# Performance work log

Hardware: AMD Instinct MI355X
Metric: run time of the kernel (lower is better)

Reference implementation:

```python
import jax, jax.numpy as jnp
import numpy as np

B, N, M = 8, 8192, 1024
C1, C2 = 256, 512
C_IN, C_MID, C_OUT = 768, 256, 256  # mlp = [768, 256, 256]
EPS_BN = 1e-5
EPS_W = 1e-8


def setup_inputs() -> dict:
    key = jax.random.key(0)
    ks = jax.random.split(key, 10)
    inp = {
        "unknown": jax.random.uniform(ks[0], (B, N, 3), dtype=jnp.float32),
        "known": jax.random.uniform(ks[1], (B, M, 3), dtype=jnp.float32),
        "unknow_feats": jax.random.normal(ks[2], (B, C1, N), dtype=jnp.float32),
        "known_feats": jax.random.normal(ks[3], (B, C2, M), dtype=jnp.float32),
        # conv1d (kernel=1) weights, bias-free (followed by BN), per create_convblock1d
        "W1": jax.random.normal(ks[4], (C_MID, C_IN), dtype=jnp.float32) * (1.0 / np.sqrt(C_IN)),
        "g1": jnp.ones((C_MID,), jnp.float32),
        "b1": jnp.zeros((C_MID,), jnp.float32),
        "W2": jax.random.normal(ks[5], (C_OUT, C_MID), dtype=jnp.float32) * (1.0 / np.sqrt(C_MID)),
        "g2": jnp.ones((C_OUT,), jnp.float32),
        "b2": jnp.zeros((C_OUT,), jnp.float32),
    }
    return inp


def _three_interpolation(unknown, known, known_feats):
    # squared pairwise distances (B, N, M), as in pointnet2 three_nn CUDA kernel
    d2 = jnp.sum((unknown[:, :, None, :] - known[:, None, :, :]) ** 2, axis=-1)
    neg_d, idx = jax.lax.top_k(-d2, 3)            # (B, N, 3)
    dist = -neg_d
    w = 1.0 / (dist + EPS_W)
    w = w / jnp.sum(w, axis=-1, keepdims=True)    # (B, N, 3)
    gathered = jax.vmap(lambda f, i: f[:, i])(known_feats, idx)  # (B, C2, N, 3)
    return jnp.einsum("bcnk,bnk->bcn", gathered, w)              # (B, C2, N)


def _conv_bn_relu(x, W, g, b):
    # 1x1 conv1d (no bias) + BatchNorm1d (training-mode stats) + ReLU
    y = jnp.einsum("oc,bcn->bon", W, x)
    mean = jnp.mean(y, axis=(0, 2), keepdims=True)
    var = jnp.var(y, axis=(0, 2), keepdims=True)
    y = (y - mean) * jax.lax.rsqrt(var + EPS_BN)
    y = y * g[None, :, None] + b[None, :, None]
    return jax.nn.relu(y)


def reference(unknown, known, unknow_feats, known_feats, W1, g1, b1, W2, g2, b2):
    interp = _three_interpolation(unknown, known, known_feats)   # (B, C2, N)
    new_features = jnp.concatenate([unknow_feats, interp], axis=1)  # (B, C1+C2, N)
    h = _conv_bn_relu(new_features, W1, g1, b1)
    out = _conv_bn_relu(h, W2, g2, b2)
    return out  # (B, C_OUT, N)
```

## Files before the change

kernel.cpp:

```cpp
#include <hip/hip_runtime.h>

#define B_    8
#define N_    8192
#define M_    1024
#define C1_   256
#define C2_   512
#define CIN_  768
#define CMID_ 256
#define COUT_ 256

typedef __attribute__((ext_vector_type(8))) __bf16 bf16x8;
typedef __attribute__((ext_vector_type(4))) float f32x4;
typedef __attribute__((ext_vector_type(4))) unsigned short u16x4;
typedef __attribute__((ext_vector_type(8))) unsigned short u16x8;

__device__ __forceinline__ unsigned short f2bf(float f) {
  union { float f; unsigned u; } v; v.f = f;
  unsigned r = v.u + 0x7FFFu + ((v.u >> 16) & 1u);
  return (unsigned short)(r >> 16);
}
__device__ __forceinline__ float bf2f(unsigned short h) {
  union { unsigned u; float f; } v; v.u = ((unsigned)h) << 16; return v.f;
}

__device__ __forceinline__ void gload16(const void* g, void* l) {
  __builtin_amdgcn_global_load_lds((const __attribute__((address_space(1))) unsigned int*)g,
                                   (__attribute__((address_space(3))) unsigned int*)l, 16, 0, 0);
}


__global__ void k_cast(const float* __restrict__ in, unsigned short* __restrict__ out, int n) {
  int i = blockIdx.x * 256 + threadIdx.x;
  if (i < n) out[i] = f2bf(in[i]);
}

__global__ void k_tr_kf(const float* __restrict__ in, float* __restrict__ out) {
  __shared__ float t[32][33];
  int b = blockIdx.z;
  int c0 = blockIdx.x * 32, m0 = blockIdx.y * 32;
  int tx = threadIdx.x, ty = threadIdx.y;
  const float* ip = in + ((size_t)b * C2_ + c0) * M_ + m0;
#pragma unroll
  for (int i = 0; i < 32; i += 8) t[ty + i][tx] = ip[(size_t)(ty + i) * M_ + tx];
  __syncthreads();
  float* op = out + ((size_t)b * M_ + m0) * C2_ + c0;
#pragma unroll
  for (int i = 0; i < 32; i += 8) op[(size_t)(ty + i) * C2_ + tx] = t[tx][ty + i];
}

__global__ void k_tr_uf(const float* __restrict__ in, unsigned short* __restrict__ out) {
  __shared__ float t[32][33];
  int b = blockIdx.z;
  int c0 = blockIdx.x * 32, n0 = blockIdx.y * 32;
  int tx = threadIdx.x, ty = threadIdx.y;
  const float* ip = in + ((size_t)b * C1_ + c0) * N_ + n0;
#pragma unroll
  for (int i = 0; i < 32; i += 8) t[ty + i][tx] = ip[(size_t)(ty + i) * N_ + tx];
  __syncthreads();
  unsigned short* op = out + ((size_t)b * N_ + n0) * CIN_ + c0;
#pragma unroll
  for (int i = 0; i < 32; i += 8) op[(size_t)(ty + i) * CIN_ + tx] = f2bf(t[tx][ty + i]);
}


__device__ __forceinline__ void ins3(float db, int ib, float& d0, int& i0,
                                     float& d1, int& i1, float& d2, int& i2) {
  if (db < d2 || (db == d2 && ib < i2)) {
    if (db < d1 || (db == d1 && ib < i1)) {
      d2 = d1; i2 = i1;
      if (db < d0 || (db == d0 && ib < i0)) { d1 = d0; i1 = i0; d0 = db; i0 = ib; }
      else                                  { d1 = db; i1 = ib; }
    } else { d2 = db; i2 = ib; }
  }
}

__global__ __launch_bounds__(256) void k_three_nn(const float* __restrict__ unknown,
                                                  const float* __restrict__ known,
                                                  int* __restrict__ idx, float* __restrict__ wgt) {
  __shared__ __align__(16) float kpts[M_][4];
  int b = blockIdx.x >> 8;
  int n0 = (blockIdx.x & 255) << 5;
  for (int i = threadIdx.x; i < M_; i += 256) {
    const float* kp = known + ((size_t)b * M_ + i) * 3;
    kpts[i][0] = kp[0]; kpts[i][1] = kp[1]; kpts[i][2] = kp[2];
  }
  __syncthreads();
  const int l = threadIdx.x & 63;
  const int j = l & 7;
  const int q = ((threadIdx.x >> 6) << 3) + (l >> 3);
  const int n = n0 + q;
  const float* up = unknown + ((size_t)b * N_ + n) * 3;
  float ux = up[0], uy = up[1], uz = up[2];
  float d0 = 1e30f, d1 = 1e30f, d2v = 1e30f;
  int i0 = 0, i1 = 0, i2 = 0;
  for (int t = 0; t < 128; ++t) {
    int i = t * 8 + j;
    f32x4 p = *(const f32x4*)kpts[i];
    float dx = __fsub_rn(ux, p[0]);
    float dy = __fsub_rn(uy, p[1]);
    float dz = __fsub_rn(uz, p[2]);
    float d = __fadd_rn(__fadd_rn(__fmul_rn(dx, dx), __fmul_rn(dy, dy)), __fmul_rn(dz, dz));
    if (d < d2v) {
      if (d < d1) {
        if (d < d0) { d2v = d1; i2 = i1; d1 = d0; i1 = i0; d0 = d; i0 = i; }
        else        { d2v = d1; i2 = i1; d1 = d;  i1 = i; }
      } else        { d2v = d;  i2 = i; }
    }
  }
#pragma unroll
  for (int m = 1; m <= 4; m <<= 1) {
    float e0 = __shfl_xor(d0, m), e1 = __shfl_xor(d1, m), e2 = __shfl_xor(d2v, m);
    int   f0 = __shfl_xor(i0, m), f1 = __shfl_xor(i1, m), f2 = __shfl_xor(i2, m);
    ins3(e0, f0, d0, i0, d1, i1, d2v, i2);
    ins3(e1, f1, d0, i0, d1, i1, d2v, i2);
    ins3(e2, f2, d0, i0, d1, i1, d2v, i2);
  }
  if (j == 0) {
    float w0 = 1.f / (d0 + 1e-8f), w1 = 1.f / (d1 + 1e-8f), w2 = 1.f / (d2v + 1e-8f);
    float s = w0 + w1 + w2;
    size_t base = ((size_t)b * N_ + n) * 3;
    idx[base] = i0; idx[base + 1] = i1; idx[base + 2] = i2;
    wgt[base] = w0 / s; wgt[base + 1] = w1 / s; wgt[base + 2] = w2 / s;
  }
}

__global__ __launch_bounds__(256) void k_interp(const float* __restrict__ kft, const int* __restrict__ idx,
                                                const float* __restrict__ wgt, unsigned short* __restrict__ xt) {
  int pb = blockIdx.x * 8 + (threadIdx.x >> 5);
  int lane = threadIdx.x & 31;
  int b = pb >> 13;
  size_t t3 = (size_t)pb * 3;
  int i0 = idx[t3], i1 = idx[t3 + 1], i2 = idx[t3 + 2];
  float w0 = wgt[t3], w1 = wgt[t3 + 1], w2 = wgt[t3 + 2];
  const f32x4* f0 = (const f32x4*)(kft + ((size_t)b * M_ + i0) * C2_);
  const f32x4* f1 = (const f32x4*)(kft + ((size_t)b * M_ + i1) * C2_);
  const f32x4* f2 = (const f32x4*)(kft + ((size_t)b * M_ + i2) * C2_);
  unsigned short* o = xt + (size_t)pb * CIN_ + C1_;
#pragma unroll
  for (int k = 0; k < 4; ++k) {
    int c4 = lane + 32 * k;
    f32x4 a = f0[c4], bb = f1[c4], cc = f2[c4];
    u16x4 r;
#pragma unroll
    for (int e = 0; e < 4; ++e) r[e] = f2bf(w0 * a[e] + w1 * bb[e] + w2 * cc[e]);
    *(u16x4*)(o + 4 * c4) = r;
  }
}


template <int K, int EPI, bool BN>
__global__ __launch_bounds__(256) void gemm_bt(const unsigned short* __restrict__ A,
                                               const unsigned short* __restrict__ Bm,
                                               unsigned short* __restrict__ C,
                                               float* __restrict__ psum, float* __restrict__ psq,
                                               const float* __restrict__ scale,
                                               const float* __restrict__ shift) {
  __shared__ __align__(16) char lds[32768];
  __shared__ float lsc[256], lsh[256];
  const int tid = threadIdx.x;
  const int l = tid & 63;
  const int wv = tid >> 6;
  const int wr = wv >> 1, wc = wv & 1;
  const int b = blockIdx.z;
  const int o0 = blockIdx.y * 128;
  const int n0 = blockIdx.x * 128;
  const char* Ab = (const char*)A + (size_t)o0 * (K * 2);
  const char* Bb = (const char*)Bm + ((size_t)b * N_ + n0) * (K * 2);

  if (BN) { lsc[tid] = scale[tid]; lsh[tid] = shift[tid]; }

  f32x4 zero = {0.f, 0.f, 0.f, 0.f};
  f32x4 acc[4][4];
#pragma unroll
  for (int i = 0; i < 4; ++i)
#pragma unroll
    for (int j = 0; j < 4; ++j) acc[i][j] = zero;

  const int grow = wv * 32 + (l >> 3);
  const int gcol = (((l & 7) ^ (l >> 3)) * 16);
  int srow[4], scol[4];
#pragma unroll
  for (int i = 0; i < 4; ++i) { int q = tid + i * 256; srow[i] = q >> 3; scol[i] = (q & 7) * 16; }

  bf16x8 rb[4];
  if (BN) {
#pragma unroll
    for (int i = 0; i < 4; ++i)
      rb[i] = *(const bf16x8*)(Bb + (size_t)srow[i] * (K * 2) + scol[i]);
  }

  const int NK = K / 64;
  for (int kt = 0; kt < NK; ++kt) {
    __syncthreads();
#pragma unroll
    for (int i = 0; i < 4; ++i) {
      int r = grow + i * 8;
      gload16(Ab + (size_t)r * (K * 2) + kt * 128 + gcol, lds + wv * 4096 + i * 1024);
      if (!BN)
        gload16(Bb + (size_t)r * (K * 2) + kt * 128 + gcol, lds + 16384 + wv * 4096 + i * 1024);
    }
    if (BN) {
#pragma unroll
      for (int i = 0; i < 4; ++i) {
        u16x8 v = *(u16x8*)&rb[i];
        u16x8 r;
        int c0 = kt * 64 + (scol[i] >> 1);
#pragma unroll
        for (int e = 0; e < 8; ++e) {
          float f = bf2f(v[e]) * lsc[c0 + e] + lsh[c0 + e];
          r[e] = f2bf(fmaxf(f, 0.f));
        }
        *(u16x8*)(lds + 16384 + srow[i] * 128 + (scol[i] ^ ((srow[i] & 7) << 4))) = r;
      }
    }
    __syncthreads();
    if (BN && kt + 1 < NK) {
      const char* Bk = Bb + (size_t)(kt + 1) * 128;
#pragma unroll
      for (int i = 0; i < 4; ++i)
        rb[i] = *(const bf16x8*)(Bk + (size_t)srow[i] * (K * 2) + scol[i]);
    }
#pragma unroll
    for (int kk = 0; kk < 2; ++kk) {
      bf16x8 af[4], bfr[4];
#pragma unroll
      for (int mi = 0; mi < 4; ++mi) {
        int row = wr * 64 + mi * 16 + (l & 15);
        int cb = (kk * 64 + ((l >> 4) * 16)) ^ ((row & 7) << 4);
        af[mi] = *(const bf16x8*)(lds + row * 128 + cb);
      }
#pragma unroll
      for (int ni = 0; ni < 4; ++ni) {
        int row = wc * 64 + ni * 16 + (l & 15);
        int cb = (kk * 64 + ((l >> 4) * 16)) ^ ((row & 7) << 4);
        bfr[ni] = *(const bf16x8*)(lds + 16384 + row * 128 + cb);
      }
#pragma unroll
      for (int mi = 0; mi < 4; ++mi)
#pragma unroll
        for (int ni = 0; ni < 4; ++ni)
          acc[mi][ni] = __builtin_amdgcn_mfma_f32_16x16x32_bf16(af[mi], bfr[ni], acc[mi][ni], 0, 0, 0);
    }
  }

#pragma unroll
  for (int mi = 0; mi < 4; ++mi) {
    int o = o0 + wr * 64 + mi * 16 + ((l >> 4) << 2);
#pragma unroll
    for (int ni = 0; ni < 4; ++ni) {
      int n = n0 + wc * 64 + ni * 16 + (l & 15);
      if (EPI == 0) {
        u16x4 pk;
#pragma unroll
        for (int r = 0; r < 4; ++r) pk[r] = f2bf(acc[mi][ni][r]);
        *(u16x4*)(C + ((size_t)b * N_ + n) * 256 + o) = pk;
      } else {
#pragma unroll
        for (int r = 0; r < 4; ++r)
          C[((size_t)b * 256 + (o + r)) * N_ + n] = f2bf(acc[mi][ni][r]);
      }
    }
  }

  const int slot = (blockIdx.z * 64 + blockIdx.x) * 2 + wc;
#pragma unroll
  for (int mi = 0; mi < 4; ++mi) {
    float s[4] = {0.f, 0.f, 0.f, 0.f}, q[4] = {0.f, 0.f, 0.f, 0.f};
#pragma unroll
    for (int ni = 0; ni < 4; ++ni)
#pragma unroll
      for (int r = 0; r < 4; ++r) { float v = acc[mi][ni][r]; s[r] += v; q[r] = fmaf(v, v, q[r]); }
#pragma unroll
    for (int m = 1; m <= 8; m <<= 1)
#pragma unroll
      for (int r = 0; r < 4; ++r) { s[r] += __shfl_xor(s[r], m); q[r] += __shfl_xor(q[r], m); }
    if ((l & 15) == 0) {
      int o = o0 + wr * 64 + mi * 16 + ((l >> 4) << 2);
#pragma unroll
      for (int r = 0; r < 4; ++r) {
        psum[(size_t)(o + r) * 1024 + slot] = s[r];
        psq [(size_t)(o + r) * 1024 + slot] = q[r];
      }
    }
  }
}


__global__ __launch_bounds__(256) void k_finalize(const float* __restrict__ psum,
                                                  const float* __restrict__ psq,
                                                  const float* __restrict__ g,
                                                  const float* __restrict__ bb,
                                                  float* __restrict__ scale,
                                                  float* __restrict__ shift) {
  int c = blockIdx.x;
  const float* ps = psum + (size_t)c * 1024;
  const float* pq = psq + (size_t)c * 1024;
  float s = 0.f, q = 0.f;
#pragma unroll
  for (int k = 0; k < 4; ++k) { s += ps[threadIdx.x + 256 * k]; q += pq[threadIdx.x + 256 * k]; }
#pragma unroll
  for (int off = 32; off; off >>= 1) { s += __shfl_down(s, off); q += __shfl_down(q, off); }
  __shared__ float rs[4], rq[4];
  if ((threadIdx.x & 63) == 0) { rs[threadIdx.x >> 6] = s; rq[threadIdx.x >> 6] = q; }
  __syncthreads();
  if (threadIdx.x == 0) {
    float S = rs[0] + rs[1] + rs[2] + rs[3];
    float Q = rq[0] + rq[1] + rq[2] + rq[3];
    const float inv_n = 1.f / 65536.f;
    float mean = S * inv_n;
    float var = Q * inv_n - mean * mean;
    float rstd = rsqrtf(var + 1e-5f);
    float sc = g[c] * rstd;
    scale[c] = sc;
    shift[c] = bb[c] - mean * sc;
  }
}

__global__ void k_bnrelu_out(const unsigned short* __restrict__ y, const float* __restrict__ scale,
                             const float* __restrict__ shift, float* __restrict__ out) {
  size_t i = ((size_t)blockIdx.x * 256 + threadIdx.x) * 4;
  int c = (int)((i >> 13) & 255);
  float sc = scale[c], sh = shift[c];
  u16x4 v = *(const u16x4*)(y + i);
  f32x4 o;
#pragma unroll
  for (int k = 0; k < 4; ++k) o[k] = fmaxf(bf2f(v[k]) * sc + sh, 0.f);
  *(f32x4*)(out + i) = o;
}


extern "C" void kernel_launch(void* const* d_in, const int* in_sizes, int n_in,
                              void* d_out, int out_size, void* d_ws, size_t ws_size,
                              hipStream_t stream) {
  const float* unknown = (const float*)d_in[0];
  const float* known   = (const float*)d_in[1];
  const float* uf      = (const float*)d_in[2];
  const float* kf      = (const float*)d_in[3];
  const float* W1      = (const float*)d_in[4];
  const float* g1      = (const float*)d_in[5];
  const float* b1      = (const float*)d_in[6];
  const float* W2      = (const float*)d_in[7];
  const float* g2      = (const float*)d_in[8];
  const float* b2      = (const float*)d_in[9];
  float* out = (float*)d_out;

  char* ws = (char*)d_ws;
  unsigned short* xt  = (unsigned short*)(ws);
  unsigned short* y1  = (unsigned short*)(ws + 100663296);
  unsigned short* y2  = (unsigned short*)(ws + 134217728);
  float*          kft = (float*)(ws + 167772160);
  float*          psum = (float*)(ws + 167772160);
  float*          psq  = (float*)(ws + 168820736);
  unsigned short* w1b = (unsigned short*)(ws + 184549376);
  unsigned short* w2b = (unsigned short*)(ws + 184942592);
  int*            idx = (int*)(ws + 185073664);
  float*          wgt = (float*)(ws + 185860096);
  float*          st  = (float*)(ws + 186646528);
  float *sc1 = st, *sh1 = st + 256, *sc2 = st + 512, *sh2 = st + 768;

  k_cast<<<768, 256, 0, stream>>>(W1, w1b, CMID_ * CIN_);
  k_cast<<<256, 256, 0, stream>>>(W2, w2b, COUT_ * CMID_);
  k_tr_kf<<<dim3(16, 32, B_), dim3(32, 8), 0, stream>>>(kf, kft);
  k_tr_uf<<<dim3(8, 256, B_), dim3(32, 8), 0, stream>>>(uf, xt);
  k_three_nn<<<B_ * 256, 256, 0, stream>>>(unknown, known, idx, wgt);
  k_interp<<<B_ * N_ / 8, 256, 0, stream>>>(kft, idx, wgt, xt);
  gemm_bt<CIN_, 0, false><<<dim3(64, 2, B_), 256, 0, stream>>>(w1b, xt, y1, psum, psq, nullptr, nullptr);
  k_finalize<<<256, 256, 0, stream>>>(psum, psq, g1, b1, sc1, sh1);
  gemm_bt<CMID_, 1, true><<<dim3(64, 2, B_), 256, 0, stream>>>(w2b, y1, y2, psum, psq, sc1, sh1);
  k_finalize<<<256, 256, 0, stream>>>(psum, psq, g2, b2, sc2, sh2);
  k_bnrelu_out<<<16384, 256, 0, stream>>>(y2, sc2, sh2, out);
}
```

Baseline: 206.0 us.

## Double-buffer LDS tiles in GEMM and stage epilogue through LDS for coalesced stores

Double-buffers the GEMM's LDS tiles so loads for the next K tile are issued before the MFMA work on the current one, leaving one barrier per iteration instead of two. BN scale and shift are now read straight from global memory as vectors instead of being staged in LDS. The output is transposed through LDS so each thread writes 16-byte rows, replacing the scattered 2-byte stores in the transposed (EPI=1) layout. LDS use doubles to 64KB, which may lower occupancy.

```diff
diff --git a/kernel.cpp b/kernel.cpp
--- a/kernel.cpp
+++ b/kernel.cpp
@@ -155,8 +155,7 @@
                                                float* __restrict__ psum, float* __restrict__ psq,
                                                const float* __restrict__ scale,
                                                const float* __restrict__ shift) {
-  __shared__ __align__(16) char lds[32768];
-  __shared__ float lsc[256], lsh[256];
+  __shared__ __align__(16) char lds[65536];
   const int tid = threadIdx.x;
   const int l = tid & 63;
   const int wv = tid >> 6;
@@ -167,8 +166,6 @@
   const char* Ab = (const char*)A + (size_t)o0 * (K * 2);
   const char* Bb = (const char*)Bm + ((size_t)b * N_ + n0) * (K * 2);
 
-  if (BN) { lsc[tid] = scale[tid]; lsh[tid] = shift[tid]; }
-
   f32x4 zero = {0.f, 0.f, 0.f, 0.f};
   f32x4 acc[4][4];
 #pragma unroll
@@ -182,44 +179,68 @@
 #pragma unroll
   for (int i = 0; i < 4; ++i) { int q = tid + i * 256; srow[i] = q >> 3; scol[i] = (q & 7) * 16; }
 
-  bf16x8 rb[4];
+  auto bnwrite = [&](bf16x8* rb, int ktv, char* dstbase) {
+#pragma unroll
+    for (int i = 0; i < 4; ++i) {
+      u16x8 v = *(u16x8*)&rb[i];
+      int c0 = ktv * 64 + (scol[i] >> 1);
+      f32x4 sa = *(const f32x4*)(scale + c0), sb = *(const f32x4*)(scale + c0 + 4);
+      f32x4 ha = *(const f32x4*)(shift + c0), hb = *(const f32x4*)(shift + c0 + 4);
+      u16x8 r;
+#pragma unroll
+      for (int e = 0; e < 4; ++e) {
+        r[e]     = f2bf(fmaxf(bf2f(v[e])     * sa[e] + ha[e], 0.f));
+        r[e + 4] = f2bf(fmaxf(bf2f(v[e + 4]) * sb[e] + hb[e], 0.f));
+      }
+      *(u16x8*)(dstbase + srow[i] * 128 + (scol[i] ^ ((srow[i] & 7) << 4))) = r;
+    }
+  };
+
   if (BN) {
+    bf16x8 rb0[4];
 #pragma unroll
     for (int i = 0; i < 4; ++i)
-      rb[i] = *(const bf16x8*)(Bb + (size_t)srow[i] * (K * 2) + scol[i]);
-  }
-
-  const int NK = K / 64;
-  for (int kt = 0; kt < NK; ++kt) {
-    __syncthreads();
+      rb0[i] = *(const bf16x8*)(Bb + (size_t)srow[i] * (K * 2) + scol[i]);
+#pragma unroll
+    for (int i = 0; i < 4; ++i)
+      gload16(Ab + (size_t)(grow + i * 8) * (K * 2) + gcol, lds + wv * 4096 + i * 1024);
+    bnwrite(rb0, 0, lds + 16384);
+  } else {
 #pragma unroll
     for (int i = 0; i < 4; ++i) {
       int r = grow + i * 8;
-      gload16(Ab + (size_t)r * (K * 2) + kt * 128 + gcol, lds + wv * 4096 + i * 1024);
-      if (!BN)
-        gload16(Bb + (size_t)r * (K * 2) + kt * 128 + gcol, lds + 16384 + wv * 4096 + i * 1024);
-    }
-    if (BN) {
-#pragma unroll
-      for (int i = 0; i < 4; ++i) {
-        u16x8 v = *(u16x8*)&rb[i];
-        u16x8 r;
-        int c0 = kt * 64 + (scol[i] >> 1);
-#pragma unroll
-        for (int e = 0; e < 8; ++e) {
-          float f = bf2f(v[e]) * lsc[c0 + e] + lsh[c0 + e];
-          r[e] = f2bf(fmaxf(f, 0.f));
+      gload16(Ab + (size_t)r * (K * 2) + gcol, lds + wv * 4096 + i * 1024);
+      gload16(Bb + (size_t)r * (K * 2) + gcol, lds + 16384 + wv * 4096 + i * 1024);
+    }
+  }
+  __syncthreads();
+
+  const int NK = K / 64;
+  int cur = 0;
+  for (int kt = 0; kt < NK; ++kt) {
+    const bool haveNext = (kt + 1 < NK);
+    bf16x8 rb2[4];
+    if (haveNext) {
+      char* nb = lds + (cur ^ 1) * 32768;
+      if (BN) {
+        const char* Bk = Bb + (size_t)(kt + 1) * 128;
+#pragma unroll
+        for (int i = 0; i < 4; ++i)
+          rb2[i] = *(const bf16x8*)(Bk + (size_t)srow[i] * (K * 2) + scol[i]);
+#pragma unroll
+        for (int i = 0; i < 4; ++i)
+          gload16(Ab + (size_t)(grow + i * 8) * (K * 2) + (kt + 1) * 128 + gcol,
+                  nb + wv * 4096 + i * 1024);
+      } else {
+#pragma unroll
+        for (int i = 0; i < 4; ++i) {
+          int r = grow + i * 8;
+          gload16(Ab + (size_t)r * (K * 2) + (kt + 1) * 128 + gcol, nb + wv * 4096 + i * 1024);
+          gload16(Bb + (size_t)r * (K * 2) + (kt + 1) * 128 + gcol, nb + 16384 + wv * 4096 + i * 1024);
         }
-        *(u16x8*)(lds + 16384 + srow[i] * 128 + (scol[i] ^ ((srow[i] & 7) << 4))) = r;
-      }
-    }
-    __syncthreads();
-    if (BN && kt + 1 < NK) {
-      const char* Bk = Bb + (size_t)(kt + 1) * 128;
-#pragma unroll
-      for (int i = 0; i < 4; ++i)
-        rb[i] = *(const bf16x8*)(Bk + (size_t)srow[i] * (K * 2) + scol[i]);
-    }
+      }
+    }
+    const char* base = lds + cur * 32768;
 #pragma unroll
     for (int kk = 0; kk < 2; ++kk) {
       bf16x8 af[4], bfr[4];
@@ -227,13 +248,13 @@
       for (int mi = 0; mi < 4; ++mi) {
         int row = wr * 64 + mi * 16 + (l & 15);
         int cb = (kk * 64 + ((l >> 4) * 16)) ^ ((row & 7) << 4);
-        af[mi] = *(const bf16x8*)(lds + row * 128 + cb);
+        af[mi] = *(const bf16x8*)(base + row * 128 + cb);
       }
 #pragma unroll
       for (int ni = 0; ni < 4; ++ni) {
         int row = wc * 64 + ni * 16 + (l & 15);
         int cb = (kk * 64 + ((l >> 4) * 16)) ^ ((row & 7) << 4);
-        bfr[ni] = *(const bf16x8*)(lds + 16384 + row * 128 + cb);
+        bfr[ni] = *(const bf16x8*)(base + 16384 + row * 128 + cb);
       }
 #pragma unroll
       for (int mi = 0; mi < 4; ++mi)
@@ -241,25 +262,9 @@
         for (int ni = 0; ni < 4; ++ni)
           acc[mi][ni] = __builtin_amdgcn_mfma_f32_16x16x32_bf16(af[mi], bfr[ni], acc[mi][ni], 0, 0, 0);
     }
-  }
-
-#pragma unroll
-  for (int mi = 0; mi < 4; ++mi) {
-    int o = o0 + wr * 64 + mi * 16 + ((l >> 4) << 2);
-#pragma unroll
-    for (int ni = 0; ni < 4; ++ni) {
-      int n = n0 + wc * 64 + ni * 16 + (l & 15);
-      if (EPI == 0) {
-        u16x4 pk;
-#pragma unroll
-        for (int r = 0; r < 4; ++r) pk[r] = f2bf(acc[mi][ni][r]);
-        *(u16x4*)(C + ((size_t)b * N_ + n) * 256 + o) = pk;
-      } else {
-#pragma unroll
-        for (int r = 0; r < 4; ++r)
-          C[((size_t)b * 256 + (o + r)) * N_ + n] = f2bf(acc[mi][ni][r]);
-      }
-    }
+    if (BN && haveNext) bnwrite(rb2, kt + 1, lds + (cur ^ 1) * 32768 + 16384);
+    __syncthreads();
+    cur ^= 1;
   }
 
   const int slot = (blockIdx.z * 64 + blockIdx.x) * 2 + wc;
@@ -282,6 +287,32 @@
         psq [(size_t)(o + r) * 1024 + slot] = q[r];
       }
     }
+  }
+
+  unsigned short* t16 = (unsigned short*)lds;
+#pragma unroll
+  for (int mi = 0; mi < 4; ++mi) {
+    int ol = wr * 64 + mi * 16 + ((l >> 4) << 2);
+#pragma unroll
+    for (int ni = 0; ni < 4; ++ni) {
+      int nl = wc * 64 + ni * 16 + (l & 15);
+#pragma unroll
+      for (int r = 0; r < 4; ++r) {
+        unsigned short v = f2bf(acc[mi][ni][r]);
+        if (EPI == 0) t16[nl * 144 + ol + r] = v;
+        else          t16[(ol + r) * 144 + nl] = v;
+      }
+    }
+  }
+  __syncthreads();
+#pragma unroll
+  for (int t = 0; t < 8; ++t) {
+    int row = wv * 32 + (l >> 4) + t * 4;
+    u16x8 v = *(const u16x8*)(t16 + row * 144 + (l & 15) * 8);
+    if (EPI == 0)
+      *(u16x8*)(C + ((size_t)b * N_ + n0 + row) * 256 + o0 + (l & 15) * 8) = v;
+    else
+      *(u16x8*)(C + ((size_t)b * 256 + o0 + row) * N_ + n0 + (l & 15) * 8) = v;
   }
 }
 
```

Measured after the change: 197.2 us. 1.04x faster.

## Rewrite 1x1-conv GEMMs as 256x256 tiles with double-buffered LDS and register-resident B

Applied to the files above, without the earlier changes.

Replaces the 128x128 GEMM with a 512-thread kernel covering all 256 output channels per block. A is double-buffered in LDS via async loads, B fragments are loaded directly into registers, and waitcnt/sched barriers plus setprio overlap loads with MFMA. BN scale/shift is applied in registers via shuffles. The second GEMM now writes point-major output, so the final BN+ReLU kernel becomes an LDS-tiled transpose. This aims to cut LDS traffic and sync stalls, but raises register pressure and halves the number of blocks.

```diff
diff --git a/kernel.cpp b/kernel.cpp
--- a/kernel.cpp
+++ b/kernel.cpp
@@ -148,123 +148,127 @@
 }
 
 
-template <int K, int EPI, bool BN>
-__global__ __launch_bounds__(256) void gemm_bt(const unsigned short* __restrict__ A,
-                                               const unsigned short* __restrict__ Bm,
-                                               unsigned short* __restrict__ C,
-                                               float* __restrict__ psum, float* __restrict__ psq,
-                                               const float* __restrict__ scale,
-                                               const float* __restrict__ shift) {
-  __shared__ __align__(16) char lds[32768];
-  __shared__ float lsc[256], lsh[256];
+template <int K, bool BN>
+__global__ __launch_bounds__(512, 2) void gemm256(const unsigned short* __restrict__ A,
+                                                  const unsigned short* __restrict__ Bm,
+                                                  unsigned short* __restrict__ C,
+                                                  float* __restrict__ psum, float* __restrict__ psq,
+                                                  const float* __restrict__ scale,
+                                                  const float* __restrict__ shift) {
+  constexpr int NK = K / 64;
+  __shared__ __align__(16) char lds[65536];
   const int tid = threadIdx.x;
   const int l = tid & 63;
   const int wv = tid >> 6;
-  const int wr = wv >> 1, wc = wv & 1;
-  const int b = blockIdx.z;
-  const int o0 = blockIdx.y * 128;
-  const int n0 = blockIdx.x * 128;
-  const char* Ab = (const char*)A + (size_t)o0 * (K * 2);
-  const char* Bb = (const char*)Bm + ((size_t)b * N_ + n0) * (K * 2);
-
-  if (BN) { lsc[tid] = scale[tid]; lsh[tid] = shift[tid]; }
-
-  f32x4 zero = {0.f, 0.f, 0.f, 0.f};
-  f32x4 acc[4][4];
-#pragma unroll
-  for (int i = 0; i < 4; ++i)
-#pragma unroll
-    for (int j = 0; j < 4; ++j) acc[i][j] = zero;
-
-  const int grow = wv * 32 + (l >> 3);
-  const int gcol = (((l & 7) ^ (l >> 3)) * 16);
-  int srow[4], scol[4];
-#pragma unroll
-  for (int i = 0; i < 4; ++i) { int q = tid + i * 256; srow[i] = q >> 3; scol[i] = (q & 7) * 16; }
-
-  bf16x8 rb[4];
+  const int wr = wv >> 2;
+  const int wc = wv & 3;
+  const int b = blockIdx.y;
+  const int n0 = blockIdx.x * 256;
+  const char* Abase = (const char*)A;
+  const char* Bbase = (const char*)Bm + ((size_t)b * N_ + n0) * (size_t)(K * 2);
+
+  f32x4 acc[8][4];
+#pragma unroll
+  for (int i = 0; i < 8; ++i)
+#pragma unroll
+    for (int j = 0; j < 4; ++j) acc[i][j] = f32x4{0.f, 0.f, 0.f, 0.f};
+
+  float scR[NK], shR[NK];
   if (BN) {
 #pragma unroll
+    for (int t = 0; t < NK; ++t) { scR[t] = scale[t * 64 + l]; shR[t] = shift[t * 64 + l]; }
+  }
+
+  const int adst = wv * 4096;
+  const size_t arow = (size_t)(wv * 32 + (l >> 3));
+  const int gcol = ((l & 7) ^ (l >> 3)) * 16;
+  const char* Brow = Bbase + (size_t)(wc * 64 + (l & 15)) * (K * 2) + (l >> 4) * 16;
+
+  auto issueA = [&](int kt, int buf) {
+#pragma unroll
     for (int i = 0; i < 4; ++i)
-      rb[i] = *(const bf16x8*)(Bb + (size_t)srow[i] * (K * 2) + scol[i]);
-  }
-
-  const int NK = K / 64;
-  for (int kt = 0; kt < NK; ++kt) {
-    __syncthreads();
-#pragma unroll
-    for (int i = 0; i < 4; ++i) {
-      int r = grow + i * 8;
-      gload16(Ab + (size_t)r * (K * 2) + kt * 128 + gcol, lds + wv * 4096 + i * 1024);
-      if (!BN)
-        gload16(Bb + (size_t)r * (K * 2) + kt * 128 + gcol, lds + 16384 + wv * 4096 + i * 1024);
-    }
+      gload16(Abase + (arow + i * 8) * (size_t)(K * 2) + kt * 128 + gcol,
+              lds + buf * 32768 + adst + i * 1024);
+  };
+  auto loadB = [&](bf16x8* bf, int kt) {
+#pragma unroll
+    for (int ni = 0; ni < 4; ++ni)
+#pragma unroll
+      for (int kk = 0; kk < 2; ++kk)
+        bf[ni * 2 + kk] = *(const bf16x8*)(Brow + (size_t)(ni * 16) * (K * 2) + kt * 128 + kk * 64);
+  };
+  auto compute = [&](int buf, bf16x8* bf, int kt) {
     if (BN) {
 #pragma unroll
-      for (int i = 0; i < 4; ++i) {
-        u16x8 v = *(u16x8*)&rb[i];
+      for (int f = 0; f < 8; ++f) {
+        int kk = f & 1;
+        u16x8 v = *(u16x8*)&bf[f];
         u16x8 r;
-        int c0 = kt * 64 + (scol[i] >> 1);
 #pragma unroll
         for (int e = 0; e < 8; ++e) {
-          float f = bf2f(v[e]) * lsc[c0 + e] + lsh[c0 + e];
-          r[e] = f2bf(fmaxf(f, 0.f));
+          int src = kk * 32 + (l >> 4) * 8 + e;
+          float sc = __shfl(scR[kt], src), sh = __shfl(shR[kt], src);
+          r[e] = f2bf(fmaxf(bf2f(v[e]) * sc + sh, 0.f));
         }
-        *(u16x8*)(lds + 16384 + srow[i] * 128 + (scol[i] ^ ((srow[i] & 7) << 4))) = r;
+        bf[f] = *(bf16x8*)&r;
       }
     }
-    __syncthreads();
-    if (BN && kt + 1 < NK) {
-      const char* Bk = Bb + (size_t)(kt + 1) * 128;
-#pragma unroll
-      for (int i = 0; i < 4; ++i)
-        rb[i] = *(const bf16x8*)(Bk + (size_t)srow[i] * (K * 2) + scol[i]);
-    }
+    const char* base = lds + buf * 32768;
+    __builtin_amdgcn_s_setprio(1);
 #pragma unroll
     for (int kk = 0; kk < 2; ++kk) {
-      bf16x8 af[4], bfr[4];
-#pragma unroll
-      for (int mi = 0; mi < 4; ++mi) {
-        int row = wr * 64 + mi * 16 + (l & 15);
-        int cb = (kk * 64 + ((l >> 4) * 16)) ^ ((row & 7) << 4);
-        af[mi] = *(const bf16x8*)(lds + row * 128 + cb);
+      bf16x8 af[8];
+#pragma unroll
+      for (int mi = 0; mi < 8; ++mi) {
+        int row = wr * 128 + mi * 16 + (l & 15);
+        int g = (kk * 4 + (l >> 4)) ^ (row & 7);
+        af[mi] = *(const bf16x8*)(base + row * 128 + g * 16);
       }
 #pragma unroll
-      for (int ni = 0; ni < 4; ++ni) {
-        int row = wc * 64 + ni * 16 + (l & 15);
-        int cb = (kk * 64 + ((l >> 4) * 16)) ^ ((row & 7) << 4);
-        bfr[ni] = *(const bf16x8*)(lds + 16384 + row * 128 + cb);
-      }
-#pragma unroll
-      for (int mi = 0; mi < 4; ++mi)
+      for (int mi = 0; mi < 8; ++mi)
 #pragma unroll
         for (int ni = 0; ni < 4; ++ni)
-          acc[mi][ni] = __builtin_amdgcn_mfma_f32_16x16x32_bf16(af[mi], bfr[ni], acc[mi][ni], 0, 0, 0);
-    }
-  }
-
-#pragma unroll
-  for (int mi = 0; mi < 4; ++mi) {
-    int o = o0 + wr * 64 + mi * 16 + ((l >> 4) << 2);
-#pragma unroll
-    for (int ni = 0; ni < 4; ++ni) {
-      int n = n0 + wc * 64 + ni * 16 + (l & 15);
-      if (EPI == 0) {
-        u16x4 pk;
-#pragma unroll
-        for (int r = 0; r < 4; ++r) pk[r] = f2bf(acc[mi][ni][r]);
-        *(u16x4*)(C + ((size_t)b * N_ + n) * 256 + o) = pk;
-      } else {
-#pragma unroll
-        for (int r = 0; r < 4; ++r)
-          C[((size_t)b * 256 + (o + r)) * N_ + n] = f2bf(acc[mi][ni][r]);
-      }
-    }
-  }
-
-  const int slot = (blockIdx.z * 64 + blockIdx.x) * 2 + wc;
-#pragma unroll
-  for (int mi = 0; mi < 4; ++mi) {
+          acc[mi][ni] = __builtin_amdgcn_mfma_f32_16x16x32_bf16(af[mi], bf[ni * 2 + kk],
+                                                                acc[mi][ni], 0, 0, 0);
+    }
+    __builtin_amdgcn_s_setprio(0);
+  };
+
+  bf16x8 bA[8], bB[8];
+  issueA(0, 0);
+  __builtin_amdgcn_sched_barrier(0);
+  loadB(bA, 0);
+  __builtin_amdgcn_sched_barrier(0);
+
+#pragma unroll
+  for (int it = 0; it < NK / 2; ++it) {
+    const int kt = 2 * it;
+    asm volatile("s_waitcnt vmcnt(8)" ::: "memory");
+    __builtin_amdgcn_s_barrier();
+    __builtin_amdgcn_sched_barrier(0);
+    if (kt + 1 < NK) {
+      issueA(kt + 1, 1);
+      __builtin_amdgcn_sched_barrier(0);
+      loadB(bB, kt + 1);
+      __builtin_amdgcn_sched_barrier(0);
+    }
+    compute(0, bA, kt);
+
+    asm volatile("s_waitcnt vmcnt(8)" ::: "memory");
+    __builtin_amdgcn_s_barrier();
+    __builtin_amdgcn_sched_barrier(0);
+    if (kt + 2 < NK) {
+      issueA(kt + 2, 0);
+      __builtin_amdgcn_sched_barrier(0);
+      loadB(bA, kt + 2);
+      __builtin_amdgcn_sched_barrier(0);
+    }
+    compute(1, bB, kt + 1);
+  }
+
+  const int slot = (b * 32 + blockIdx.x) * 4 + wc;
+#pragma unroll
+  for (int mi = 0; mi < 8; ++mi) {
     float s[4] = {0.f, 0.f, 0.f, 0.f}, q[4] = {0.f, 0.f, 0.f, 0.f};
 #pragma unroll
     for (int ni = 0; ni < 4; ++ni)
@@ -275,12 +279,25 @@
 #pragma unroll
       for (int r = 0; r < 4; ++r) { s[r] += __shfl_xor(s[r], m); q[r] += __shfl_xor(q[r], m); }
     if ((l & 15) == 0) {
-      int o = o0 + wr * 64 + mi * 16 + ((l >> 4) << 2);
+      int o = wr * 128 + mi * 16 + ((l >> 4) << 2);
 #pragma unroll
       for (int r = 0; r < 4; ++r) {
         psum[(size_t)(o + r) * 1024 + slot] = s[r];
         psq [(size_t)(o + r) * 1024 + slot] = q[r];
       }
+    }
+  }
+
+#pragma unroll
+  for (int mi = 0; mi < 8; ++mi) {
+    int o = wr * 128 + mi * 16 + ((l >> 4) << 2);
+#pragma unroll
+    for (int ni = 0; ni < 4; ++ni) {
+      int n = n0 + wc * 64 + ni * 16 + (l & 15);
+      u16x4 pk;
+#pragma unroll
+      for (int r = 0; r < 4; ++r) pk[r] = f2bf(acc[mi][ni][r]);
+      *(u16x4*)(C + ((size_t)b * N_ + n) * 256 + o) = pk;
     }
   }
 }
@@ -316,16 +333,22 @@
   }
 }
 
-__global__ void k_bnrelu_out(const unsigned short* __restrict__ y, const float* __restrict__ scale,
-                             const float* __restrict__ shift, float* __restrict__ out) {
-  size_t i = ((size_t)blockIdx.x * 256 + threadIdx.x) * 4;
-  int c = (int)((i >> 13) & 255);
-  float sc = scale[c], sh = shift[c];
-  u16x4 v = *(const u16x4*)(y + i);
-  f32x4 o;
-#pragma unroll
-  for (int k = 0; k < 4; ++k) o[k] = fmaxf(bf2f(v[k]) * sc + sh, 0.f);
-  *(f32x4*)(out + i) = o;
+__global__ void k_trbnout(const unsigned short* __restrict__ y, const float* __restrict__ scale,
+                          const float* __restrict__ shift, float* __restrict__ out) {
+  __shared__ float t[32][33];
+  int b = blockIdx.z;
+  int n0 = blockIdx.x * 32, c0 = blockIdx.y * 32;
+  int tx = threadIdx.x, ty = threadIdx.y;
+  float sc = scale[c0 + tx], sh = shift[c0 + tx];
+#pragma unroll
+  for (int i = 0; i < 32; i += 8) {
+    float v = bf2f(y[((size_t)b * N_ + n0 + ty + i) * 256 + c0 + tx]);
+    t[ty + i][tx] = fmaxf(v * sc + sh, 0.f);
+  }
+  __syncthreads();
+  float* op = out + ((size_t)b * 256 + c0) * N_ + n0;
+#pragma unroll
+  for (int i = 0; i < 32; i += 8) op[(size_t)(ty + i) * N_ + tx] = t[tx][ty + i];
 }
 
 
@@ -364,9 +387,9 @@
   k_tr_uf<<<dim3(8, 256, B_), dim3(32, 8), 0, stream>>>(uf, xt);
   k_three_nn<<<B_ * 256, 256, 0, stream>>>(unknown, known, idx, wgt);
   k_interp<<<B_ * N_ / 8, 256, 0, stream>>>(kft, idx, wgt, xt);
-  gemm_bt<CIN_, 0, false><<<dim3(64, 2, B_), 256, 0, stream>>>(w1b, xt, y1, psum, psq, nullptr, nullptr);
+  gemm256<CIN_, false><<<dim3(32, B_), 512, 0, stream>>>(w1b, xt, y1, psum, psq, nullptr, nullptr);
   k_finalize<<<256, 256, 0, stream>>>(psum, psq, g1, b1, sc1, sh1);
-  gemm_bt<CMID_, 1, true><<<dim3(64, 2, B_), 256, 0, stream>>>(w2b, y1, y2, psum, psq, sc1, sh1);
+  gemm256<CMID_, true><<<dim3(32, B_), 512, 0, stream>>>(w2b, y1, y2, psum, psq, sc1, sh1);
   k_finalize<<<256, 256, 0, stream>>>(psum, psq, g2, b2, sc2, sh2);
-  k_bnrelu_out<<<16384, 256, 0, stream>>>(y2, sc2, sh2, out);
-}
+  k_trbnout<<<dim3(256, 8, B_), dim3(32, 8), 0, stream>>>(y2, sc2, sh2, out);
+}
```

After: 238.4 us. 1.16x slower.
